# Kernel optimization log

Measured on AMD Instinct MI355X. Metric: run time of the kernel, lower is better.

The kernel has to match this reference:

```python
import jax, jax.numpy as jnp
import numpy as np


def setup_inputs() -> dict:
    key = jax.random.key(0)
    kZ, kQ, kW, kU, kbk = jax.random.split(key, 5)
    B, E, D = 64, 16, 64
    N_ATOMS = 200000
    N_NP = 160000
    N_BK = 20000
    Q_DIM = 64
    Z = jax.random.normal(kZ, (B, E, D), dtype=jnp.float32)
    Q = jax.random.normal(kQ, (B, Q_DIM), dtype=jnp.float32)
    W = jax.random.normal(kW, (N_NP, D), dtype=jnp.float32)
    U = jax.random.normal(kU, (N_NP, Q_DIM), dtype=jnp.float32)
    np_indices = jnp.arange(N_NP, dtype=jnp.int64 if jax.config.jax_enable_x64 else jnp.int32)
    bk_indices = jax.random.randint(kbk, (N_BK,), 0, N_ATOMS, dtype=jnp.int32)
    return {"Z": Z, "Q": Q, "W": W, "U": U,
            "np_indices": np_indices, "bk_indices": bk_indices,
            "n_atoms": N_ATOMS}


def reference(Z, Q, W, U, np_indices, bk_indices, n_atoms):
    # Batched valuation for all neural-predicate atoms at once:
    # vm(Z, Q, atom_i) = sigmoid(sum_{e,d} Z[b,e,d] * W[i,d] + Q[b] . U[i])
    scores = jax.nn.sigmoid(jnp.einsum('bed,nd->bn', Z, W) + Q @ U.T)  # [B, n_np]
    B = Z.shape[0]
    V = jnp.zeros((B, n_atoms), dtype=jnp.float32)
    V = V.at[:, 0].set(1.0)                 # V[:, 0] = 1.0 (true atom)
    V = V.at[:, np_indices].set(scores)     # scatter valuation outputs
    V = V.at[:, bk_indices].add(1.0)        # background knowledge atoms += 1
    return V
```

## Files before the change

kernel.cpp:

```cpp
#include <hip/hip_runtime.h>


typedef _Float16 half8_t __attribute__((ext_vector_type(8)));
typedef float float4_t __attribute__((ext_vector_type(4)));

#define E_DIM 16
#define D_DIM 64
#define QD    64
#define NS    4
#define ET_STRIDE 68

__global__ void prep_kernel(const float* __restrict__ Z, const float* __restrict__ Q,
                            const int* __restrict__ bk, int n_bk,
                            _Float16* __restrict__ Afrag, float* __restrict__ cnt) {
    int blk = blockIdx.x;
    int tid = threadIdx.x;
    if (blk < 32) {
        int t = blk * 256 + tid;
        int b = t >> 7, k = t & 127;
        float v;
        if (k < D_DIM) {
            const float* zp = Z + (size_t)b * E_DIM * D_DIM + k;
            v = 0.f;
            #pragma unroll
            for (int e = 0; e < E_DIM; ++e) v += zp[e * D_DIM];
        } else {
            v = Q[b * QD + (k - D_DIM)];
        }
        int mt = b >> 4, r = b & 15;
        int kq = k >> 5, j = k & 7, quad = (k >> 3) & 3;
        int lane = r + quad * 16;
        Afrag[(((mt * 4 + kq) * 64) + lane) * 8 + j] = (_Float16)v;
    } else if (cnt) {
        int i = (blk - 32) * 256 + tid;
        if (i < n_bk) atomicAdd(&cnt[bk[i]], 1.0f);
    }
}

__global__ __launch_bounds__(256) void main_kernel(
        const float* __restrict__ W, const float* __restrict__ U,
        const _Float16* __restrict__ Afrag, const float* __restrict__ cnt,
        float* __restrict__ V, int n_np, int n_atoms, int n_gemm_blocks) {
    __shared__ __align__(16) float eT[2][64][ET_STRIDE];
    int tid = threadIdx.x;
    int bid = blockIdx.x;
    int c  = tid & 15;
    int rr = tid >> 4;

    if (bid >= n_gemm_blocks) {
        long long nblk = (long long)n_np + (long long)(bid - n_gemm_blocks) * 64;
        float4_t cn4 = {0.f, 0.f, 0.f, 0.f};
        if (cnt) cn4 = *(const float4_t*)(cnt + nblk + 4 * c);
        #pragma unroll
        for (int p = 0; p < 4; ++p) {
            int row = p * 16 + rr;
            *(float4_t*)(V + (size_t)row * n_atoms + nblk + 4 * c) = cn4;
        }
        return;
    }

    long long base = (long long)bid * (64 * NS);
    int wv = tid >> 6, lane = tid & 63;
    int quad = lane >> 4, l15 = lane & 15;
    int rB = wv * 16 + l15;

    const half8_t* Ap = (const half8_t*)Afrag;
    half8_t a[4][4];
    #pragma unroll
    for (int mt = 0; mt < 4; ++mt)
        #pragma unroll
        for (int kq = 0; kq < 4; ++kq)
            a[mt][kq] = Ap[(mt * 4 + kq) * 64 + lane];

    const float4_t* Wg = (const float4_t*)W;
    const float4_t* Ug = (const float4_t*)U;

    float4_t wb[2][4], ub[2][4];
    auto load_strip = [&](int s, float4_t wr[4], float4_t ur[4]) {
        size_t o = ((size_t)(base + s * 64 + rB)) * 16 + quad * 2;
        wr[0] = Wg[o];     wr[1] = Wg[o + 1];
        wr[2] = Wg[o + 8]; wr[3] = Wg[o + 9];
        ur[0] = Ug[o];     ur[1] = Ug[o + 1];
        ur[2] = Ug[o + 8]; ur[3] = Ug[o + 9];
    };

    load_strip(0, wb[0], ub[0]);

    #pragma unroll
    for (int s = 0; s < NS; ++s) {
        if (s + 1 < NS) load_strip(s + 1, wb[(s + 1) & 1], ub[(s + 1) & 1]);

        float4_t cn4 = {0.f, 0.f, 0.f, 0.f};
        if (cnt) cn4 = *(const float4_t*)(cnt + base + s * 64 + 4 * c);

        half8_t b0, b1, b2, b3;
        #pragma unroll
        for (int q = 0; q < 4; ++q) {
            b0[q]     = (_Float16)wb[s & 1][0][q];
            b0[q + 4] = (_Float16)wb[s & 1][1][q];
            b1[q]     = (_Float16)wb[s & 1][2][q];
            b1[q + 4] = (_Float16)wb[s & 1][3][q];
            b2[q]     = (_Float16)ub[s & 1][0][q];
            b2[q + 4] = (_Float16)ub[s & 1][1][q];
            b3[q]     = (_Float16)ub[s & 1][2][q];
            b3[q + 4] = (_Float16)ub[s & 1][3][q];
        }

        float4_t acc[4] = {{0.f,0.f,0.f,0.f},{0.f,0.f,0.f,0.f},
                           {0.f,0.f,0.f,0.f},{0.f,0.f,0.f,0.f}};
        #pragma unroll
        for (int mt = 0; mt < 4; ++mt) {
            acc[mt] = __builtin_amdgcn_mfma_f32_16x16x32_f16(a[mt][0], b0, acc[mt], 0, 0, 0);
            acc[mt] = __builtin_amdgcn_mfma_f32_16x16x32_f16(a[mt][1], b1, acc[mt], 0, 0, 0);
            acc[mt] = __builtin_amdgcn_mfma_f32_16x16x32_f16(a[mt][2], b2, acc[mt], 0, 0, 0);
            acc[mt] = __builtin_amdgcn_mfma_f32_16x16x32_f16(a[mt][3], b3, acc[mt], 0, 0, 0);
        }

        #pragma unroll
        for (int mt = 0; mt < 4; ++mt)
            #pragma unroll
            for (int r = 0; r < 4; ++r)
                eT[s & 1][mt * 16 + quad * 4 + r][wv * 16 + l15] = acc[mt][r];
        __syncthreads();

        long long nblk = base + s * 64;
        #pragma unroll
        for (int p = 0; p < 4; ++p) {
            int row = p * 16 + rr;
            float4_t v = *(const float4_t*)&eT[s & 1][row][4 * c];
            float4_t out;
            #pragma unroll
            for (int q = 0; q < 4; ++q)
                out[q] = 1.0f / (1.0f + __expf(-v[q])) + cn4[q];
            *(float4_t*)(V + (size_t)row * n_atoms + nblk + 4 * c) = out;
        }
    }
}

__global__ void bk_scatter(const int* __restrict__ bk, int n_bk,
                           float* __restrict__ V, int n_atoms) {
    int i = blockIdx.x * 256 + threadIdx.x;
    if (i < n_bk)
        atomicAdd(&V[(size_t)blockIdx.y * n_atoms + bk[i]], 1.0f);
}

extern "C" void kernel_launch(void* const* d_in, const int* in_sizes, int n_in,
                              void* d_out, int out_size, void* d_ws, size_t ws_size,
                              hipStream_t stream) {
    const float* Z = (const float*)d_in[0];
    const float* Q = (const float*)d_in[1];
    const float* W = (const float*)d_in[2];
    const float* U = (const float*)d_in[3];
    const int* bk = (const int*)d_in[5];
    float* V = (float*)d_out;

    int B       = in_sizes[0] / (E_DIM * D_DIM);
    int n_np    = in_sizes[2] / D_DIM;
    int n_bk    = in_sizes[5];
    int n_atoms = out_size / B;

    _Float16* Afrag = (_Float16*)d_ws;
    size_t need = 16384 + (size_t)n_atoms * sizeof(float);
    bool use_cnt = ws_size >= need;
    float* cnt = use_cnt ? (float*)((char*)d_ws + 16384) : nullptr;

    if (use_cnt) {
        hipMemsetAsync(cnt, 0, (size_t)n_atoms * sizeof(float), stream);
        int cnt_blocks = (n_bk + 255) / 256;
        prep_kernel<<<32 + cnt_blocks, 256, 0, stream>>>(Z, Q, bk, n_bk, Afrag, cnt);
    } else {
        prep_kernel<<<32, 256, 0, stream>>>(Z, Q, bk, n_bk, Afrag, nullptr);
    }

    int gb = n_np / (64 * NS);
    int tail_blocks = (n_atoms - n_np) / 64;
    main_kernel<<<gb + tail_blocks, 256, 0, stream>>>(W, U, Afrag, cnt, V,
                                                      n_np, n_atoms, gb);

    if (!use_cnt) {
        dim3 g((n_bk + 255) / 256, B);
        bk_scatter<<<g, 256, 0, stream>>>(bk, n_bk, V, n_atoms);
    }
}
```

Baseline: 140.5 us.

## Drop LDS transpose, stream A fragments, fold tail into GEMM blocks

The main kernel now writes each sigmoid result straight from the MFMA accumulator layout to global memory, which removes the shared-memory transpose and its __syncthreads. The A fragments are reloaded through volatile loads inside the loop rather than held in registers, and launch bounds request 4 blocks per CU to raise occupancy. Strips per block drop from 4 to 2, and the zero/count tail region is spread across the GEMM blocks instead of using separate tail blocks. In exchange, the stores become scalar 4-byte writes with 16-column contiguity rather than float4 row writes, and the A fragments are re-read repeatedly.

```diff
diff --git a/kernel.cpp b/kernel.cpp
--- a/kernel.cpp
+++ b/kernel.cpp
@@ -7,8 +7,7 @@
 #define E_DIM 16
 #define D_DIM 64
 #define QD    64
-#define NS    4
-#define ET_STRIDE 68
+#define NS    2
 
 __global__ void prep_kernel(const float* __restrict__ Z, const float* __restrict__ Q,
                             const int* __restrict__ bk, int n_bk,
@@ -37,102 +36,87 @@
     }
 }
 
-__global__ __launch_bounds__(256) void main_kernel(
+__global__ __launch_bounds__(256, 4) void main_kernel(
         const float* __restrict__ W, const float* __restrict__ U,
         const _Float16* __restrict__ Afrag, const float* __restrict__ cnt,
-        float* __restrict__ V, int n_np, int n_atoms, int n_gemm_blocks) {
-    __shared__ __align__(16) float eT[2][64][ET_STRIDE];
+        float* __restrict__ V, int n_np, int n_atoms, int tail_w) {
     int tid = threadIdx.x;
     int bid = blockIdx.x;
-    int c  = tid & 15;
-    int rr = tid >> 4;
-
-    if (bid >= n_gemm_blocks) {
-        long long nblk = (long long)n_np + (long long)(bid - n_gemm_blocks) * 64;
-        float4_t cn4 = {0.f, 0.f, 0.f, 0.f};
-        if (cnt) cn4 = *(const float4_t*)(cnt + nblk + 4 * c);
-        #pragma unroll
-        for (int p = 0; p < 4; ++p) {
-            int row = p * 16 + rr;
-            *(float4_t*)(V + (size_t)row * n_atoms + nblk + 4 * c) = cn4;
-        }
-        return;
-    }
-
     long long base = (long long)bid * (64 * NS);
     int wv = tid >> 6, lane = tid & 63;
     int quad = lane >> 4, l15 = lane & 15;
     int rB = wv * 16 + l15;
 
-    const half8_t* Ap = (const half8_t*)Afrag;
-    half8_t a[4][4];
-    #pragma unroll
-    for (int mt = 0; mt < 4; ++mt)
-        #pragma unroll
-        for (int kq = 0; kq < 4; ++kq)
-            a[mt][kq] = Ap[(mt * 4 + kq) * 64 + lane];
-
     const float4_t* Wg = (const float4_t*)W;
     const float4_t* Ug = (const float4_t*)U;
+    const volatile half8_t* Ap = (const volatile half8_t*)Afrag;
 
-    float4_t wb[2][4], ub[2][4];
-    auto load_strip = [&](int s, float4_t wr[4], float4_t ur[4]) {
-        size_t o = ((size_t)(base + s * 64 + rB)) * 16 + quad * 2;
-        wr[0] = Wg[o];     wr[1] = Wg[o + 1];
-        wr[2] = Wg[o + 8]; wr[3] = Wg[o + 9];
-        ur[0] = Ug[o];     ur[1] = Ug[o + 1];
-        ur[2] = Ug[o + 8]; ur[3] = Ug[o + 9];
-    };
+    float4_t wraw[4], uraw[4];
+    {
+        size_t o = ((size_t)(base + rB)) * 16 + quad * 2;
+        wraw[0] = Wg[o];     wraw[1] = Wg[o + 1];
+        wraw[2] = Wg[o + 8]; wraw[3] = Wg[o + 9];
+        uraw[0] = Ug[o];     uraw[1] = Ug[o + 1];
+        uraw[2] = Ug[o + 8]; uraw[3] = Ug[o + 9];
+    }
 
-    load_strip(0, wb[0], ub[0]);
+    {
+        long long tb = (long long)n_np + (long long)bid * tail_w;
+        int c8 = tid & 7, rg = tid >> 3;
+        long long col = tb + 4 * c8;
+        if (4 * c8 < tail_w && col < n_atoms) {
+            float4_t cn4 = {0.f, 0.f, 0.f, 0.f};
+            if (cnt) cn4 = *(const float4_t*)(cnt + col);
+            *(float4_t*)(V + (size_t)rg * n_atoms + col) = cn4;
+            *(float4_t*)(V + (size_t)(rg + 32) * n_atoms + col) = cn4;
+        }
+    }
 
     #pragma unroll
     for (int s = 0; s < NS; ++s) {
-        if (s + 1 < NS) load_strip(s + 1, wb[(s + 1) & 1], ub[(s + 1) & 1]);
+        long long colbase = base + s * 64;
 
-        float4_t cn4 = {0.f, 0.f, 0.f, 0.f};
-        if (cnt) cn4 = *(const float4_t*)(cnt + base + s * 64 + 4 * c);
+        float cn = 0.f;
+        if (cnt) cn = cnt[colbase + rB];
 
         half8_t b0, b1, b2, b3;
         #pragma unroll
         for (int q = 0; q < 4; ++q) {
-            b0[q]     = (_Float16)wb[s & 1][0][q];
-            b0[q + 4] = (_Float16)wb[s & 1][1][q];
-            b1[q]     = (_Float16)wb[s & 1][2][q];
-            b1[q + 4] = (_Float16)wb[s & 1][3][q];
-            b2[q]     = (_Float16)ub[s & 1][0][q];
-            b2[q + 4] = (_Float16)ub[s & 1][1][q];
-            b3[q]     = (_Float16)ub[s & 1][2][q];
-            b3[q + 4] = (_Float16)ub[s & 1][3][q];
+            b0[q]     = (_Float16)wraw[0][q];
+            b0[q + 4] = (_Float16)wraw[1][q];
+            b1[q]     = (_Float16)wraw[2][q];
+            b1[q + 4] = (_Float16)wraw[3][q];
+            b2[q]     = (_Float16)uraw[0][q];
+            b2[q + 4] = (_Float16)uraw[1][q];
+            b3[q]     = (_Float16)uraw[2][q];
+            b3[q + 4] = (_Float16)uraw[3][q];
         }
 
-        float4_t acc[4] = {{0.f,0.f,0.f,0.f},{0.f,0.f,0.f,0.f},
-                           {0.f,0.f,0.f,0.f},{0.f,0.f,0.f,0.f}};
-        #pragma unroll
-        for (int mt = 0; mt < 4; ++mt) {
-            acc[mt] = __builtin_amdgcn_mfma_f32_16x16x32_f16(a[mt][0], b0, acc[mt], 0, 0, 0);
-            acc[mt] = __builtin_amdgcn_mfma_f32_16x16x32_f16(a[mt][1], b1, acc[mt], 0, 0, 0);
-            acc[mt] = __builtin_amdgcn_mfma_f32_16x16x32_f16(a[mt][2], b2, acc[mt], 0, 0, 0);
-            acc[mt] = __builtin_amdgcn_mfma_f32_16x16x32_f16(a[mt][3], b3, acc[mt], 0, 0, 0);
+        if (s + 1 < NS) {
+            size_t o = ((size_t)(base + (s + 1) * 64 + rB)) * 16 + quad * 2;
+            wraw[0] = Wg[o];     wraw[1] = Wg[o + 1];
+            wraw[2] = Wg[o + 8]; wraw[3] = Wg[o + 9];
+            uraw[0] = Ug[o];     uraw[1] = Ug[o + 1];
+            uraw[2] = Ug[o + 8]; uraw[3] = Ug[o + 9];
         }
 
         #pragma unroll
-        for (int mt = 0; mt < 4; ++mt)
+        for (int mt = 0; mt < 4; ++mt) {
+            half8_t a0 = Ap[(mt * 4 + 0) * 64 + lane];
+            half8_t a1 = Ap[(mt * 4 + 1) * 64 + lane];
+            half8_t a2 = Ap[(mt * 4 + 2) * 64 + lane];
+            half8_t a3 = Ap[(mt * 4 + 3) * 64 + lane];
+            float4_t acc = {0.f, 0.f, 0.f, 0.f};
+            acc = __builtin_amdgcn_mfma_f32_16x16x32_f16(a0, b0, acc, 0, 0, 0);
+            acc = __builtin_amdgcn_mfma_f32_16x16x32_f16(a1, b1, acc, 0, 0, 0);
+            acc = __builtin_amdgcn_mfma_f32_16x16x32_f16(a2, b2, acc, 0, 0, 0);
+            acc = __builtin_amdgcn_mfma_f32_16x16x32_f16(a3, b3, acc, 0, 0, 0);
+            float* vp = V + (size_t)(mt * 16 + quad * 4) * n_atoms + colbase + rB;
             #pragma unroll
-            for (int r = 0; r < 4; ++r)
-                eT[s & 1][mt * 16 + quad * 4 + r][wv * 16 + l15] = acc[mt][r];
-        __syncthreads();
-
-        long long nblk = base + s * 64;
-        #pragma unroll
-        for (int p = 0; p < 4; ++p) {
-            int row = p * 16 + rr;
-            float4_t v = *(const float4_t*)&eT[s & 1][row][4 * c];
-            float4_t out;
-            #pragma unroll
-            for (int q = 0; q < 4; ++q)
-                out[q] = 1.0f / (1.0f + __expf(-v[q])) + cn4[q];
-            *(float4_t*)(V + (size_t)row * n_atoms + nblk + 4 * c) = out;
+            for (int r = 0; r < 4; ++r) {
+                float sv = 1.0f / (1.0f + __expf(-acc[r])) + cn;
+                vp[(size_t)r * n_atoms] = sv;
+            }
         }
     }
 }
@@ -173,9 +157,9 @@
     }
 
     int gb = n_np / (64 * NS);
-    int tail_blocks = (n_atoms - n_np) / 64;
-    main_kernel<<<gb + tail_blocks, 256, 0, stream>>>(W, U, Afrag, cnt, V,
-                                                      n_np, n_atoms, gb);
+    int tail_w = (n_atoms - n_np + gb - 1) / gb;
+    main_kernel<<<gb, 256, 0, stream>>>(W, U, Afrag, cnt, V,
+                                        n_np, n_atoms, tail_w);
 
     if (!use_cnt) {
         dim3 g((n_bk + 255) / 256, B);
```

Result: slower. 148.0 us (+5.3%).
